# Performance work log

Hardware: AMD Instinct MI355X
Metric: run time of the kernel (lower is better)

## Reference

```python
import jax, jax.numpy as jnp
import numpy as np

STATE_DIM = 32
OBS_DIM = 16
PROCESS_VAR = 1e-4
MEAS_VAR = 1e-2
B = 2048
T = 64


def setup_inputs() -> dict:
    key = jax.random.key(0)
    k1, k2, k3 = jax.random.split(key, 3)
    state0 = jax.random.normal(k1, (B, STATE_DIM), dtype=jnp.float32)
    # Initial covariance P = I (per torch __init__), broadcast over batch
    cov0 = jnp.broadcast_to(jnp.eye(STATE_DIM, dtype=jnp.float32), (B, STATE_DIM, STATE_DIM))
    measurements = jax.random.normal(k2, (B, T, OBS_DIM), dtype=jnp.float32)
    # Parameters per torch __init__: F = eye, H = randn, Q = pv*I, R = mv*I
    F = jnp.eye(STATE_DIM, dtype=jnp.float32)
    H = jax.random.normal(k3, (OBS_DIM, STATE_DIM), dtype=jnp.float32)
    Q = PROCESS_VAR * jnp.eye(STATE_DIM, dtype=jnp.float32)
    R = MEAS_VAR * jnp.eye(OBS_DIM, dtype=jnp.float32)
    return {"state0": state0, "cov0": cov0, "measurements": measurements,
            "F": F, "H": H, "Q": Q, "R": R}


def reference(state0, cov0, measurements, F, H, Q, R):
    """Run Kalman predict+update over T timesteps; return filtered states (B,T,S)."""

    def step(carry, z):
        x, P = carry  # x: (B,S), P: (B,S,S); z: (B,O)
        # --- predict ---
        x_pred = x @ F.T                                   # F @ x per batch
        P_pred = jnp.einsum('ij,bjk,lk->bil', F, P, F) + Q  # F P F^T + Q
        # --- update ---
        y = x_pred @ H.T                                   # predicted measurement (B,O)
        innov = z - y
        S = jnp.einsum('ij,bjk,lk->bil', H, P_pred, H) + R  # (B,O,O)
        S_inv = jnp.linalg.inv(S)
        K = jnp.einsum('bij,kj,bkl->bil', P_pred, H, S_inv)  # P H^T S^{-1}, (B,S,O)
        x_new = x_pred + jnp.einsum('bij,bj->bi', K, innov)
        P_new = P_pred - jnp.einsum('bij,jk,bkl->bil', K, H, P_pred)  # (I - K H) P
        return (x_new, P_new), x_new

    # scan over time axis: measurements (B,T,O) -> (T,B,O)
    (_, _), states = jax.lax.scan(step, (state0, cov0), jnp.swapaxes(measurements, 0, 1))
    return jnp.swapaxes(states, 0, 1)  # (B,T,S)
```

## Files before the change

kernel.cpp:

```cpp
#include <hip/hip_runtime.h>
#include <math.h>


#define S_DIM 32
#define O_DIM 16
#define K_STRIDE 512
#define HS 36
#define CW 8

typedef unsigned int u32;

__device__ __forceinline__ float rdlanef(float v, int srcLane) {
    return __uint_as_float(
        (unsigned int)__builtin_amdgcn_readlane((int)__float_as_uint(v), srcLane));
}

__global__ __launch_bounds__(512) void fused_kernel(
    const float* __restrict__ state0,
    const float* __restrict__ cov0,
    const float* __restrict__ meas,
    const float* __restrict__ Fm,
    const float* __restrict__ Hm,
    const float* __restrict__ Qm,
    const float* __restrict__ Rm,
    float* __restrict__ wsK,
    float* __restrict__ out,
    int T, int B)
{
    u32* ctrl = (u32*)(wsK + (long)T * K_STRIDE);
    const int tid = threadIdx.x;

    __shared__ float P  [S_DIM*33];
    __shared__ float Fs [S_DIM*33];
    __shared__ float Qs [S_DIM*33];
    __shared__ float Tp [S_DIM*33];
    __shared__ float Hs [O_DIM*HS];
    __shared__ float HQ [O_DIM*HS];
    __shared__ float HPs[O_DIM*HS];
    __shared__ float KT [O_DIM*33];
    __shared__ float Sg [O_DIM*17];
    __shared__ float Rs [O_DIM*17];
    __shared__ int notId, notDiag, convFlag, convT;
    __shared__ float Ks[K_STRIDE];
    __shared__ float xs[CW][32];
    __shared__ float iv[CW][16];
    __shared__ u32 mail;

    if (blockIdx.x == 0) {
        for (int i = tid; i < S_DIM*S_DIM; i += 512) {
            int r = i >> 5, c = i & 31;
            P [r*33+c] = cov0[i];
            Fs[r*33+c] = Fm[i];
            Qs[r*33+c] = Qm[i];
        }
        for (int i = tid; i < O_DIM*S_DIM; i += 512) {
            int r = i >> 5, c = i & 31;
            Hs[r*HS+c] = Hm[i];
        }
        for (int i = tid; i < O_DIM*O_DIM; i += 512) {
            int r = i >> 4, c = i & 15;
            Rs[r*17+c] = Rm[i];
        }
        if (tid == 0) { notId = 0; notDiag = 0; convFlag = 0; convT = 0; }
        __syncthreads();

        {
            bool badI = false, badD = false;
            for (int i = tid; i < S_DIM*S_DIM; i += 512) {
                int r = i >> 5, c = i & 31;
                if (Fs[r*33+c] != ((r == c) ? 1.0f : 0.0f)) badI = true;
            }
            for (int i = tid; i < O_DIM*O_DIM; i += 512) {
                int r = i >> 4, c = i & 15;
                if (r != c && Rs[r*17+c] != 0.0f) badD = true;
            }
            if (badI) notId = 1;
            if (badD) notDiag = 1;
        }
        __syncthreads();
        const bool fId   = (notId == 0);
        const bool rDiag = (notDiag == 0);

        if (tid < 64) __builtin_amdgcn_s_setprio(1);

        if (fId) {
            for (int i = tid; i < S_DIM*S_DIM; i += 512) {
                int r = i >> 5, c = i & 31;
                P[r*33+c] += Qs[r*33+c];
            }
        }
        __syncthreads();

        if (fId) {
            int r = tid >> 5, c = tid & 31;
            float a0 = 0.f, q0 = 0.f;
            for (int k = 0; k < S_DIM; ++k) {
                a0 += Hs[r*HS+k]*P [k*33+c];
                q0 += Hs[r*HS+k]*Qs[k*33+c];
            }
            HPs[r*HS+c] = a0;
            HQ [r*HS+c] = q0;
        }
        __syncthreads();

        bool  havePend = false;
        int   pendT = 0;
        float4 pf0, pf1, pf2, pf3;
        float prevK[16];

        for (int t = 0; t < T; ++t) {
            if (havePend) {
                float4* dst = (float4*)(wsK + (long)pendT*K_STRIDE + (tid - O_DIM)*O_DIM);
                dst[0] = pf0; dst[1] = pf1; dst[2] = pf2; dst[3] = pf3;
                havePend = false;
            }

            if (!fId) {
                for (int i = tid; i < S_DIM*S_DIM; i += 512) {
                    int r = i >> 5, c = i & 31;
                    float a = 0.f;
                    for (int k = 0; k < S_DIM; ++k) a += Fs[r*33+k]*P[k*33+c];
                    Tp[r*33+c] = a;
                }
                __syncthreads();
                for (int i = tid; i < S_DIM*S_DIM; i += 512) {
                    int r = i >> 5, c = i & 31;
                    float a = Qs[r*33+c];
                    for (int k = 0; k < S_DIM; ++k) a += Tp[r*33+k]*Fs[c*33+k];
                    P[r*33+c] = a;
                }
                __syncthreads();
                {
                    int r = tid >> 5, c = tid & 31;
                    float a = 0.f;
                    for (int k = 0; k < S_DIM; ++k)
                        a += Hs[r*HS+k]*P[k*33+c];
                    HPs[r*HS+c] = a;
                }
                __syncthreads();
            }

            if (tid < 256) {
                int r = tid >> 4, c = tid & 15;
                float a = Rs[r*17+c];
                const float4* hp = (const float4*)&HPs[r*HS];
                const float4* hh = (const float4*)&Hs [c*HS];
                #pragma unroll
                for (int k = 0; k < 8; ++k) {
                    float4 u = hp[k], v = hh[k];
                    a += u.x*v.x + u.y*v.y + u.z*v.z + u.w*v.w;
                }
                Sg[r*17+c] = a;
            }
            __syncthreads();

            if (tid == 511 && t > 0)
                __hip_atomic_store(ctrl, (u32)t, __ATOMIC_RELEASE,
                                   __HIP_MEMORY_SCOPE_AGENT);

            if (tid < 64) {
                const int myc = tid;
                const bool isS = (myc < O_DIM);
                const bool isK = (!isS && myc < 48);
                const int hc = (myc - O_DIM) & 31;
                float a[16];
                #pragma unroll
                for (int r = 0; r < O_DIM; ++r)
                    a[r] = isS ? Sg[r*17+myc] : HPs[r*HS+hc];

                #pragma unroll
                for (int p = 0; p < O_DIM; ++p) {
                    float sp[16];
                    #pragma unroll
                    for (int r = 0; r < O_DIM; ++r) sp[r] = rdlanef(a[r], p);
                    float pinv = __builtin_amdgcn_rcpf(sp[p]);
                    float sc = a[p] * pinv;
                    #pragma unroll
                    for (int r = 0; r < O_DIM; ++r)
                        a[r] = (r == p) ? sc : fmaf(-sp[r], sc, a[r]);
                }

                float d = 0.f;
                if (isK) {
                    #pragma unroll
                    for (int r = 0; r < O_DIM; ++r) {
                        float dd = fabsf(a[r] - prevK[r]);
                        d = fmaxf(d, dd);
                        prevK[r] = a[r];
                    }
                }
                unsigned long long anyBig = __ballot(isK && (d > 1e-5f));
                if (myc == 0 && anyBig == 0ull && t >= 1) {
                    convFlag = 1; convT = t;
                }

                if (isK) {
                    pf0 = make_float4(a[0],  a[1],  a[2],  a[3]);
                    pf1 = make_float4(a[4],  a[5],  a[6],  a[7]);
                    pf2 = make_float4(a[8],  a[9],  a[10], a[11]);
                    pf3 = make_float4(a[12], a[13], a[14], a[15]);
                    pendT = t; havePend = true;

                    const int j = myc - O_DIM;
                    if (fId) {
                        if (rDiag) {
                            #pragma unroll
                            for (int r = 0; r < O_DIM; ++r)
                                HPs[r*HS+j] = fmaf(Rs[r*17+r], a[r], HQ[r*HS+j]);
                        } else {
                            #pragma unroll
                            for (int r = 0; r < O_DIM; ++r) {
                                float rg = 0.f;
                                for (int k = 0; k < O_DIM; ++k) rg += Rs[r*17+k]*a[k];
                                HPs[r*HS+j] = rg + HQ[r*HS+j];
                            }
                        }
                    } else {
                        #pragma unroll
                        for (int o = 0; o < O_DIM; ++o) KT[o*33+j] = a[o];
                    }
                }
            }
            __syncthreads();

            if (convFlag) break;

            if (!fId) {
                for (int i = tid; i < S_DIM*S_DIM; i += 512) {
                    int r = i >> 5, c = i & 31;
                    float acc = 0.f;
                    for (int o = 0; o < O_DIM; ++o) acc += KT[o*33+r]*HPs[o*HS+c];
                    P[r*33+c] -= acc;
                }
                __syncthreads();
            }
        }

        if (havePend) {
            float4* dst = (float4*)(wsK + (long)pendT*K_STRIDE + (tid - O_DIM)*O_DIM);
            dst[0] = pf0; dst[1] = pf1; dst[2] = pf2; dst[3] = pf3;
        }
        __syncthreads();

        if (!fId && convFlag) {
            const int tc = convT;
            const long n = (long)(T - 1 - tc) * K_STRIDE;
            const float* src = wsK + (long)tc * K_STRIDE;
            float* dst = wsK + (long)(tc + 1) * K_STRIDE;
            for (long i = tid; i < n; i += 512)
                dst[i] = src[i & (K_STRIDE - 1)];
            __syncthreads();
        }

        if (tid == 0) {
            u32 tsv = (convFlag && fId) ? (u32)convT : (u32)T;
            __hip_atomic_store(ctrl, (tsv << 16) | (u32)T, __ATOMIC_RELEASE,
                               __HIP_MEMORY_SCOPE_AGENT);
        }
        return;
    }

    const int wv = tid >> 6;
    const int l  = tid & 63;
    const int s = l & 31;
    const int h = l >> 5;
    const int o = l & 15;
    const int q = l >> 4;
    long bb = (long)(blockIdx.x - 1) * CW + wv;
    const long b = (bb < B) ? bb : (B - 1);

    float4 h0v, h1v;
    {
        const float4* Hv = (const float4*)(Hm + o*S_DIM + q*8);
        h0v = Hv[0]; h1v = Hv[1];
    }

    bool bad = false;
    for (int i = l; i < S_DIM*S_DIM; i += 64) {
        int r = i >> 5, c = i & 31;
        if (Fm[i] != ((r == c) ? 1.0f : 0.0f)) bad = true;
    }
    const bool fId = !__any(bad);

    float4 f0, f1, f2, f3;
    if (!fId) {
        const float4* Fv = (const float4*)(Fm + s*S_DIM + h*16);
        f0 = Fv[0]; f1 = Fv[1]; f2 = Fv[2]; f3 = Fv[3];
    }

    float x = state0[b*S_DIM + s];
    if (h == 0) xs[wv][s] = x;
    __builtin_amdgcn_wave_barrier();

    int t = 0, avail = 0, ts = 0;
    while (t < T) {
        if (avail <= t && !(ts != 0 && t >= ts)) {
            for (;;) {
                __syncthreads();
                if (tid == 0)
                    mail = __hip_atomic_load(ctrl, __ATOMIC_RELAXED,
                                             __HIP_MEMORY_SCOPE_AGENT);
                __syncthreads();
                u32 cw = mail;
                avail = (int)(cw & 0xFFFFu);
                ts    = (int)(cw >> 16);
                if (avail > t || (ts != 0 && t >= ts)) break;
                __builtin_amdgcn_s_sleep(8);
            }
        }
        if (ts != 0 && t >= ts) break;

        int upto = avail;
        if (ts != 0 && ts < upto) upto = ts;
        if (upto > T) upto = T;

        for (; t < upto; ++t) {
            Ks[tid] = __hip_atomic_load(wsK + (long)t*K_STRIDE + tid,
                                        __ATOMIC_RELAXED, __HIP_MEMORY_SCOPE_AGENT);
            __syncthreads();

            float za = meas[(b*T + t)*O_DIM + o];

            if (!fId) {
                const float4* xv = (const float4*)(&xs[wv][h*16]);
                float4 xa = xv[0], xb = xv[1], xc = xv[2], xd = xv[3];
                float p = f0.x*xa.x + f0.y*xa.y + f0.z*xa.z + f0.w*xa.w
                        + f1.x*xb.x + f1.y*xb.y + f1.z*xb.z + f1.w*xb.w
                        + f2.x*xc.x + f2.y*xc.y + f2.z*xc.z + f2.w*xc.w
                        + f3.x*xd.x + f3.y*xd.y + f3.z*xd.z + f3.w*xd.w;
                x = p + __shfl_xor(p, 32, 64);
                __builtin_amdgcn_wave_barrier();
                if (h == 0) xs[wv][s] = x;
                __builtin_amdgcn_wave_barrier();
            }

            const float4* xq = (const float4*)(&xs[wv][q*8]);
            float4 xa = xq[0], xb = xq[1];
            float p = h0v.x*xa.x + h0v.y*xa.y + h0v.z*xa.z + h0v.w*xa.w
                    + h1v.x*xb.x + h1v.y*xb.y + h1v.z*xb.z + h1v.w*xb.w;
            float p2 = p + __shfl_xor(p, 16, 64);
            float y  = p2 + __shfl_xor(p2, 32, 64);
            float innov = za - y;

            __builtin_amdgcn_wave_barrier();
            if (l < 16) iv[wv][o] = innov;
            __builtin_amdgcn_wave_barrier();

            const float4* Kv = (const float4*)(&Ks[s*O_DIM + h*8]);
            float4 k0 = Kv[0], k1 = Kv[1];
            const float4* ivq = (const float4*)(&iv[wv][h*8]);
            float4 va = ivq[0], vb = ivq[1];
            float xp2 = k0.x*va.x + k0.y*va.y + k0.z*va.z + k0.w*va.w
                      + k1.x*vb.x + k1.y*vb.y + k1.z*vb.z + k1.w*vb.w;
            float xnew = x + (xp2 + __shfl_xor(xp2, 32, 64));

            if (h == 0) out[(b*T + t)*S_DIM + s] = xnew;

            __builtin_amdgcn_wave_barrier();
            if (h == 0) xs[wv][s] = xnew;
            __builtin_amdgcn_wave_barrier();

            x = xnew;
            __syncthreads();
        }
    }

    if (t >= T) return;

    Ks[tid] = __hip_atomic_load(wsK + (long)ts*K_STRIDE + tid,
                                __ATOMIC_RELAXED, __HIP_MEMORY_SCOPE_AGENT);
    __syncthreads();

    float ka[16];
    #pragma unroll
    for (int j = 0; j < 16; ++j) ka[j] = Ks[s*O_DIM + j];

    float4 kc0, kc1;
    kc0.x = h ? ka[8]  : ka[0];  kc0.y = h ? ka[9]  : ka[1];
    kc0.z = h ? ka[10] : ka[2];  kc0.w = h ? ka[11] : ka[3];
    kc1.x = h ? ka[12] : ka[4];  kc1.y = h ? ka[13] : ka[5];
    kc1.z = h ? ka[14] : ka[6];  kc1.w = h ? ka[15] : ka[7];

    float mreg[16];
    #pragma unroll
    for (int j = 0; j < 16; ++j)
        mreg[j] = (s == h*16 + j) ? 1.0f : 0.0f;
    for (int oo = 0; oo < O_DIM; ++oo) {
        const float4* Hr = (const float4*)(Hm + oo*S_DIM + h*16);
        float4 a0 = Hr[0], a1 = Hr[1], a2 = Hr[2], a3 = Hr[3];
        float k = ka[oo];
        mreg[0]  = fmaf(-k, a0.x, mreg[0]);
        mreg[1]  = fmaf(-k, a0.y, mreg[1]);
        mreg[2]  = fmaf(-k, a0.z, mreg[2]);
        mreg[3]  = fmaf(-k, a0.w, mreg[3]);
        mreg[4]  = fmaf(-k, a1.x, mreg[4]);
        mreg[5]  = fmaf(-k, a1.y, mreg[5]);
        mreg[6]  = fmaf(-k, a1.z, mreg[6]);
        mreg[7]  = fmaf(-k, a1.w, mreg[7]);
        mreg[8]  = fmaf(-k, a2.x, mreg[8]);
        mreg[9]  = fmaf(-k, a2.y, mreg[9]);
        mreg[10] = fmaf(-k, a2.z, mreg[10]);
        mreg[11] = fmaf(-k, a2.w, mreg[11]);
        mreg[12] = fmaf(-k, a3.x, mreg[12]);
        mreg[13] = fmaf(-k, a3.y, mreg[13]);
        mreg[14] = fmaf(-k, a3.z, mreg[14]);
        mreg[15] = fmaf(-k, a3.w, mreg[15]);
    }

    float4 zva0, zva1, zvb0, zvb1;
    {
        const float4* Zv = (const float4*)(meas + (b*T + t)*O_DIM + h*8);
        zva0 = Zv[0]; zva1 = Zv[1];
        const int t1 = (t + 1 < T) ? (t + 1) : t;
        const float4* Zv1 = (const float4*)(meas + (b*T + t1)*O_DIM + h*8);
        zvb0 = Zv1[0]; zvb1 = Zv1[1];
    }

    for (; t < T; ++t) {
        float4 zvc0, zvc1;
        {
            const int tn = (t + 2 < T) ? (t + 2) : (T - 1);
            const float4* Zv = (const float4*)(meas + (b*T + tn)*O_DIM + h*8);
            zvc0 = Zv[0]; zvc1 = Zv[1];
        }

        const float4* xv = (const float4*)(&xs[wv][h*16]);
        float4 xa = xv[0], xb = xv[1], xc = xv[2], xd = xv[3];
        float p = mreg[0] *xa.x + mreg[1] *xa.y + mreg[2] *xa.z + mreg[3] *xa.w
                + mreg[4] *xb.x + mreg[5] *xb.y + mreg[6] *xb.z + mreg[7] *xb.w
                + mreg[8] *xc.x + mreg[9] *xc.y + mreg[10]*xc.z + mreg[11]*xc.w
                + mreg[12]*xd.x + mreg[13]*xd.y + mreg[14]*xd.z + mreg[15]*xd.w;
        p += kc0.x*zva0.x + kc0.y*zva0.y + kc0.z*zva0.z + kc0.w*zva0.w
           + kc1.x*zva1.x + kc1.y*zva1.y + kc1.z*zva1.z + kc1.w*zva1.w;
        float xnew = p + __shfl_xor(p, 32, 64);

        if (h == 0) out[(b*T + t)*S_DIM + s] = xnew;

        __builtin_amdgcn_wave_barrier();
        if (h == 0) xs[wv][s] = xnew;
        __builtin_amdgcn_wave_barrier();

        zva0 = zvb0; zva1 = zvb1;
        zvb0 = zvc0; zvb1 = zvc1;
    }
}

extern "C" void kernel_launch(void* const* d_in, const int* in_sizes, int n_in,
                              void* d_out, int out_size, void* d_ws, size_t ws_size,
                              hipStream_t stream) {
    const float* state0 = (const float*)d_in[0];
    const float* cov0   = (const float*)d_in[1];
    const float* meas   = (const float*)d_in[2];
    const float* Fm     = (const float*)d_in[3];
    const float* Hm     = (const float*)d_in[4];
    const float* Qm     = (const float*)d_in[5];
    const float* Rm     = (const float*)d_in[6];
    float* out  = (float*)d_out;
    float* wsK  = (float*)d_ws;

    const int B = in_sizes[0] / S_DIM;
    const int T = in_sizes[2] / (B * O_DIM);

    hipMemsetAsync((void*)(wsK + (long)T * K_STRIDE), 0, sizeof(unsigned int), stream);

    const int grid = 1 + (B + CW - 1) / CW;
    fused_kernel<<<dim3(grid), dim3(512), 0, stream>>>(
        state0, cov0, meas, Fm, Hm, Qm, Rm, wsK, out, T, B);
}
```

Baseline: 152.4 us.

## Add dedicated writer wave for gain publishing and widen consumer blocks to nine columns

```diff
diff --git a/kernel.cpp b/kernel.cpp
--- a/kernel.cpp
+++ b/kernel.cpp
@@ -6,16 +6,22 @@
 #define O_DIM 16
 #define K_STRIDE 512
 #define HS 36
-#define CW 8
+#define CW 9
+#define NTHR 576
 
 typedef unsigned int u32;
+typedef unsigned long long u64;
 
 __device__ __forceinline__ float rdlanef(float v, int srcLane) {
     return __uint_as_float(
         (unsigned int)__builtin_amdgcn_readlane((int)__float_as_uint(v), srcLane));
 }
 
-__global__ __launch_bounds__(512) void fused_kernel(
+__device__ __forceinline__ u64 pack2(float a, float b) {
+    return (u64)__float_as_uint(a) | ((u64)__float_as_uint(b) << 32);
+}
+
+__global__ __launch_bounds__(NTHR) void fused_kernel(
     const float* __restrict__ state0,
     const float* __restrict__ cov0,
     const float* __restrict__ meas,
@@ -47,17 +53,17 @@
     __shared__ u32 mail;
 
     if (blockIdx.x == 0) {
-        for (int i = tid; i < S_DIM*S_DIM; i += 512) {
+        for (int i = tid; i < S_DIM*S_DIM; i += NTHR) {
             int r = i >> 5, c = i & 31;
             P [r*33+c] = cov0[i];
             Fs[r*33+c] = Fm[i];
             Qs[r*33+c] = Qm[i];
         }
-        for (int i = tid; i < O_DIM*S_DIM; i += 512) {
+        for (int i = tid; i < O_DIM*S_DIM; i += NTHR) {
             int r = i >> 5, c = i & 31;
             Hs[r*HS+c] = Hm[i];
         }
-        for (int i = tid; i < O_DIM*O_DIM; i += 512) {
+        for (int i = tid; i < O_DIM*O_DIM; i += NTHR) {
             int r = i >> 4, c = i & 15;
             Rs[r*17+c] = Rm[i];
         }
@@ -66,11 +72,11 @@
 
         {
             bool badI = false, badD = false;
-            for (int i = tid; i < S_DIM*S_DIM; i += 512) {
+            for (int i = tid; i < S_DIM*S_DIM; i += NTHR) {
                 int r = i >> 5, c = i & 31;
                 if (Fs[r*33+c] != ((r == c) ? 1.0f : 0.0f)) badI = true;
             }
-            for (int i = tid; i < O_DIM*O_DIM; i += 512) {
+            for (int i = tid; i < O_DIM*O_DIM; i += NTHR) {
                 int r = i >> 4, c = i & 15;
                 if (r != c && Rs[r*17+c] != 0.0f) badD = true;
             }
@@ -84,14 +90,14 @@
         if (tid < 64) __builtin_amdgcn_s_setprio(1);
 
         if (fId) {
-            for (int i = tid; i < S_DIM*S_DIM; i += 512) {
+            for (int i = tid; i < S_DIM*S_DIM; i += NTHR) {
                 int r = i >> 5, c = i & 31;
                 P[r*33+c] += Qs[r*33+c];
             }
         }
         __syncthreads();
 
-        if (fId) {
+        if (fId && tid < 512) {
             int r = tid >> 5, c = tid & 31;
             float a0 = 0.f, q0 = 0.f;
             for (int k = 0; k < S_DIM; ++k) {
@@ -103,34 +109,42 @@
         }
         __syncthreads();
 
-        bool  havePend = false;
-        int   pendT = 0;
-        float4 pf0, pf1, pf2, pf3;
         float prevK[16];
 
         for (int t = 0; t < T; ++t) {
-            if (havePend) {
-                float4* dst = (float4*)(wsK + (long)pendT*K_STRIDE + (tid - O_DIM)*O_DIM);
-                dst[0] = pf0; dst[1] = pf1; dst[2] = pf2; dst[3] = pf3;
-                havePend = false;
+            if (t > 0 && tid >= 512 && tid < 544) {
+                const int j = tid - 512;
+                float k0=KT[0*33+j], k1=KT[1*33+j], k2=KT[2*33+j], k3=KT[3*33+j];
+                float k4=KT[4*33+j], k5=KT[5*33+j], k6=KT[6*33+j], k7=KT[7*33+j];
+                float k8=KT[8*33+j], k9=KT[9*33+j], kA=KT[10*33+j], kB=KT[11*33+j];
+                float kC=KT[12*33+j], kD=KT[13*33+j], kE=KT[14*33+j], kF=KT[15*33+j];
+                u64* dst = (u64*)(wsK + (long)(t-1)*K_STRIDE + j*O_DIM);
+                __hip_atomic_store(dst+0, pack2(k0,k1), __ATOMIC_RELAXED, __HIP_MEMORY_SCOPE_AGENT);
+                __hip_atomic_store(dst+1, pack2(k2,k3), __ATOMIC_RELAXED, __HIP_MEMORY_SCOPE_AGENT);
+                __hip_atomic_store(dst+2, pack2(k4,k5), __ATOMIC_RELAXED, __HIP_MEMORY_SCOPE_AGENT);
+                __hip_atomic_store(dst+3, pack2(k6,k7), __ATOMIC_RELAXED, __HIP_MEMORY_SCOPE_AGENT);
+                __hip_atomic_store(dst+4, pack2(k8,k9), __ATOMIC_RELAXED, __HIP_MEMORY_SCOPE_AGENT);
+                __hip_atomic_store(dst+5, pack2(kA,kB), __ATOMIC_RELAXED, __HIP_MEMORY_SCOPE_AGENT);
+                __hip_atomic_store(dst+6, pack2(kC,kD), __ATOMIC_RELAXED, __HIP_MEMORY_SCOPE_AGENT);
+                __hip_atomic_store(dst+7, pack2(kE,kF), __ATOMIC_RELAXED, __HIP_MEMORY_SCOPE_AGENT);
             }
 
             if (!fId) {
-                for (int i = tid; i < S_DIM*S_DIM; i += 512) {
+                for (int i = tid; i < S_DIM*S_DIM; i += NTHR) {
                     int r = i >> 5, c = i & 31;
                     float a = 0.f;
                     for (int k = 0; k < S_DIM; ++k) a += Fs[r*33+k]*P[k*33+c];
                     Tp[r*33+c] = a;
                 }
                 __syncthreads();
-                for (int i = tid; i < S_DIM*S_DIM; i += 512) {
+                for (int i = tid; i < S_DIM*S_DIM; i += NTHR) {
                     int r = i >> 5, c = i & 31;
                     float a = Qs[r*33+c];
                     for (int k = 0; k < S_DIM; ++k) a += Tp[r*33+k]*Fs[c*33+k];
                     P[r*33+c] = a;
                 }
                 __syncthreads();
-                {
+                if (tid < 512) {
                     int r = tid >> 5, c = tid & 31;
                     float a = 0.f;
                     for (int k = 0; k < S_DIM; ++k)
@@ -154,8 +168,8 @@
             }
             __syncthreads();
 
-            if (tid == 511 && t > 0)
-                __hip_atomic_store(ctrl, (u32)t, __ATOMIC_RELEASE,
+            if (tid == 575 && t > 0)
+                __hip_atomic_store(ctrl, (u32)t, __ATOMIC_RELAXED,
                                    __HIP_MEMORY_SCOPE_AGENT);
 
             if (tid < 64) {
@@ -195,13 +209,10 @@
                 }
 
                 if (isK) {
-                    pf0 = make_float4(a[0],  a[1],  a[2],  a[3]);
-                    pf1 = make_float4(a[4],  a[5],  a[6],  a[7]);
-                    pf2 = make_float4(a[8],  a[9],  a[10], a[11]);
-                    pf3 = make_float4(a[12], a[13], a[14], a[15]);
-                    pendT = t; havePend = true;
-
                     const int j = myc - O_DIM;
+                    #pragma unroll
+                    for (int o = 0; o < O_DIM; ++o) KT[o*33+j] = a[o];
+
                     if (fId) {
                         if (rDiag) {
                             #pragma unroll
@@ -215,9 +226,6 @@
                                 HPs[r*HS+j] = rg + HQ[r*HS+j];
                             }
                         }
-                    } else {
-                        #pragma unroll
-                        for (int o = 0; o < O_DIM; ++o) KT[o*33+j] = a[o];
                     }
                 }
             }
@@ -226,7 +234,7 @@
             if (convFlag) break;
 
             if (!fId) {
-                for (int i = tid; i < S_DIM*S_DIM; i += 512) {
+                for (int i = tid; i < S_DIM*S_DIM; i += NTHR) {
                     int r = i >> 5, c = i & 31;
                     float acc = 0.f;
                     for (int o = 0; o < O_DIM; ++o) acc += KT[o*33+r]*HPs[o*HS+c];
@@ -236,9 +244,24 @@
             }
         }
 
-        if (havePend) {
-            float4* dst = (float4*)(wsK + (long)pendT*K_STRIDE + (tid - O_DIM)*O_DIM);
-            dst[0] = pf0; dst[1] = pf1; dst[2] = pf2; dst[3] = pf3;
+        {
+            const int tLast = convFlag ? convT : (T - 1);
+            if (tid >= 512 && tid < 544) {
+                const int j = tid - 512;
+                float k0=KT[0*33+j], k1=KT[1*33+j], k2=KT[2*33+j], k3=KT[3*33+j];
+                float k4=KT[4*33+j], k5=KT[5*33+j], k6=KT[6*33+j], k7=KT[7*33+j];
+                float k8=KT[8*33+j], k9=KT[9*33+j], kA=KT[10*33+j], kB=KT[11*33+j];
+                float kC=KT[12*33+j], kD=KT[13*33+j], kE=KT[14*33+j], kF=KT[15*33+j];
+                u64* dst = (u64*)(wsK + (long)tLast*K_STRIDE + j*O_DIM);
+                __hip_atomic_store(dst+0, pack2(k0,k1), __ATOMIC_RELAXED, __HIP_MEMORY_SCOPE_AGENT);
+                __hip_atomic_store(dst+1, pack2(k2,k3), __ATOMIC_RELAXED, __HIP_MEMORY_SCOPE_AGENT);
+                __hip_atomic_store(dst+2, pack2(k4,k5), __ATOMIC_RELAXED, __HIP_MEMORY_SCOPE_AGENT);
+                __hip_atomic_store(dst+3, pack2(k6,k7), __ATOMIC_RELAXED, __HIP_MEMORY_SCOPE_AGENT);
+                __hip_atomic_store(dst+4, pack2(k8,k9), __ATOMIC_RELAXED, __HIP_MEMORY_SCOPE_AGENT);
+                __hip_atomic_store(dst+5, pack2(kA,kB), __ATOMIC_RELAXED, __HIP_MEMORY_SCOPE_AGENT);
+                __hip_atomic_store(dst+6, pack2(kC,kD), __ATOMIC_RELAXED, __HIP_MEMORY_SCOPE_AGENT);
+                __hip_atomic_store(dst+7, pack2(kE,kF), __ATOMIC_RELAXED, __HIP_MEMORY_SCOPE_AGENT);
+            }
         }
         __syncthreads();
 
@@ -247,7 +270,7 @@
             const long n = (long)(T - 1 - tc) * K_STRIDE;
             const float* src = wsK + (long)tc * K_STRIDE;
             float* dst = wsK + (long)(tc + 1) * K_STRIDE;
-            for (long i = tid; i < n; i += 512)
+            for (long i = tid; i < n; i += NTHR)
                 dst[i] = src[i & (K_STRIDE - 1)];
             __syncthreads();
         }
@@ -315,8 +338,9 @@
         if (upto > T) upto = T;
 
         for (; t < upto; ++t) {
-            Ks[tid] = __hip_atomic_load(wsK + (long)t*K_STRIDE + tid,
-                                        __ATOMIC_RELAXED, __HIP_MEMORY_SCOPE_AGENT);
+            if (tid < 512)
+                Ks[tid] = __hip_atomic_load(wsK + (long)t*K_STRIDE + tid,
+                                            __ATOMIC_RELAXED, __HIP_MEMORY_SCOPE_AGENT);
             __syncthreads();
 
             float za = meas[(b*T + t)*O_DIM + o];
@@ -367,8 +391,9 @@
 
     if (t >= T) return;
 
-    Ks[tid] = __hip_atomic_load(wsK + (long)ts*K_STRIDE + tid,
-                                __ATOMIC_RELAXED, __HIP_MEMORY_SCOPE_AGENT);
+    if (tid < 512)
+        Ks[tid] = __hip_atomic_load(wsK + (long)ts*K_STRIDE + tid,
+                                    __ATOMIC_RELAXED, __HIP_MEMORY_SCOPE_AGENT);
     __syncthreads();
 
     float ka[16];
@@ -464,6 +489,6 @@
     hipMemsetAsync((void*)(wsK + (long)T * K_STRIDE), 0, sizeof(unsigned int), stream);
 
     const int grid = 1 + (B + CW - 1) / CW;
-    fused_kernel<<<dim3(grid), dim3(512), 0, stream>>>(
+    fused_kernel<<<dim3(grid), dim3(NTHR), 53248, stream>>>(
         state0, cov0, meas, Fm, Hm, Qm, Rm, wsK, out, T, B);
 }
```

Result: faster. 144.0 us (-5.5%).

## Compute covariance recursion redundantly per block instead of broadcasting gain via global memory

Applied to the files above, without the earlier changes.

```diff
diff --git a/kernel.cpp b/kernel.cpp
--- a/kernel.cpp
+++ b/kernel.cpp
@@ -4,18 +4,16 @@
 
 #define S_DIM 32
 #define O_DIM 16
-#define K_STRIDE 512
 #define HS 36
 #define CW 8
-
-typedef unsigned int u32;
+#define NTHR 576
 
 __device__ __forceinline__ float rdlanef(float v, int srcLane) {
     return __uint_as_float(
         (unsigned int)__builtin_amdgcn_readlane((int)__float_as_uint(v), srcLane));
 }
 
-__global__ __launch_bounds__(512) void fused_kernel(
+__global__ __launch_bounds__(NTHR) void kf_fused(
     const float* __restrict__ state0,
     const float* __restrict__ cov0,
     const float* __restrict__ meas,
@@ -23,11 +21,9 @@
     const float* __restrict__ Hm,
     const float* __restrict__ Qm,
     const float* __restrict__ Rm,
-    float* __restrict__ wsK,
     float* __restrict__ out,
     int T, int B)
 {
-    u32* ctrl = (u32*)(wsK + (long)T * K_STRIDE);
     const int tid = threadIdx.x;
 
     __shared__ float P  [S_DIM*33];
@@ -37,61 +33,108 @@
     __shared__ float Hs [O_DIM*HS];
     __shared__ float HQ [O_DIM*HS];
     __shared__ float HPs[O_DIM*HS];
-    __shared__ float KT [O_DIM*33];
+    __shared__ float KT [2][O_DIM*33];
     __shared__ float Sg [O_DIM*17];
     __shared__ float Rs [O_DIM*17];
+    __shared__ float xs [CW][32];
+    __shared__ float iv [CW][16];
     __shared__ int notId, notDiag, convFlag, convT;
-    __shared__ float Ks[K_STRIDE];
-    __shared__ float xs[CW][32];
-    __shared__ float iv[CW][16];
-    __shared__ u32 mail;
-
-    if (blockIdx.x == 0) {
-        for (int i = tid; i < S_DIM*S_DIM; i += 512) {
+    __shared__ float cupad[13000];
+
+    if (tid == 0) {
+        ((volatile float*)cupad)[0] = 0.f;
+        notId = 0; notDiag = 0; convFlag = 0; convT = 0;
+    }
+
+    for (int i = tid; i < S_DIM*S_DIM; i += NTHR) {
+        int r = i >> 5, c = i & 31;
+        P [r*33+c] = cov0[i];
+        Fs[r*33+c] = Fm[i];
+        Qs[r*33+c] = Qm[i];
+    }
+    for (int i = tid; i < O_DIM*S_DIM; i += NTHR) {
+        int r = i >> 5, c = i & 31;
+        Hs[r*HS+c] = Hm[i];
+    }
+    for (int i = tid; i < O_DIM*O_DIM; i += NTHR) {
+        int r = i >> 4, c = i & 15;
+        Rs[r*17+c] = Rm[i];
+    }
+    __syncthreads();
+
+    {
+        bool badI = false, badD = false;
+        for (int i = tid; i < S_DIM*S_DIM; i += NTHR) {
             int r = i >> 5, c = i & 31;
-            P [r*33+c] = cov0[i];
-            Fs[r*33+c] = Fm[i];
-            Qs[r*33+c] = Qm[i];
-        }
-        for (int i = tid; i < O_DIM*S_DIM; i += 512) {
+            if (Fs[r*33+c] != ((r == c) ? 1.0f : 0.0f)) badI = true;
+        }
+        for (int i = tid; i < O_DIM*O_DIM; i += NTHR) {
+            int r = i >> 4, c = i & 15;
+            if (r != c && Rs[r*17+c] != 0.0f) badD = true;
+        }
+        if (badI) notId = 1;
+        if (badD) notDiag = 1;
+    }
+    __syncthreads();
+    const bool fId   = (notId == 0);
+    const bool rDiag = (notDiag == 0);
+
+    const int wv = tid >> 6;
+    const int l  = tid & 63;
+    const int s  = l & 31;
+    const int h  = l >> 5;
+    const int o  = l & 15;
+    const int q  = l >> 4;
+    const int wi = (wv >= 1) ? (wv - 1) : 0;
+    const bool isCons = (wv >= 1);
+    long bb = (long)blockIdx.x * CW + wi;
+    const long b = (bb < B) ? bb : (B - 1);
+
+    float4 h0v, h1v;
+    {
+        const float4* Hv = (const float4*)(Hm + o*S_DIM + q*8);
+        h0v = Hv[0]; h1v = Hv[1];
+    }
+
+    float x = 0.f;
+    if (isCons) {
+        x = state0[b*S_DIM + s];
+        if (h == 0) xs[wi][s] = x;
+    }
+    __syncthreads();
+
+    auto cons_step = [&](int tstep, int bufc) {
+        float za = meas[(b*T + tstep)*O_DIM + o];
+        const float4* xq = (const float4*)(&xs[wi][q*8]);
+        float4 xa = xq[0], xb = xq[1];
+        float p = h0v.x*xa.x + h0v.y*xa.y + h0v.z*xa.z + h0v.w*xa.w
+                + h1v.x*xb.x + h1v.y*xb.y + h1v.z*xb.z + h1v.w*xb.w;
+        float p2 = p + __shfl_xor(p, 16, 64);
+        float y  = p2 + __shfl_xor(p2, 32, 64);
+        float innov = za - y;
+        __builtin_amdgcn_wave_barrier();
+        if (l < 16) iv[wi][o] = innov;
+        __builtin_amdgcn_wave_barrier();
+        const float* ivp = &iv[wi][h*8];
+        const float* ktp = &KT[bufc][(h*8)*33 + s];
+        float acc = 0.f;
+        #pragma unroll
+        for (int m = 0; m < 8; ++m) acc = fmaf(ktp[m*33], ivp[m], acc);
+        float xnew = x + (acc + __shfl_xor(acc, 32, 64));
+        if (h == 0) out[(b*T + tstep)*S_DIM + s] = xnew;
+        __builtin_amdgcn_wave_barrier();
+        if (h == 0) xs[wi][s] = xnew;
+        __builtin_amdgcn_wave_barrier();
+        x = xnew;
+    };
+
+    if (fId) {
+        for (int i = tid; i < S_DIM*S_DIM; i += NTHR) {
             int r = i >> 5, c = i & 31;
-            Hs[r*HS+c] = Hm[i];
-        }
-        for (int i = tid; i < O_DIM*O_DIM; i += 512) {
-            int r = i >> 4, c = i & 15;
-            Rs[r*17+c] = Rm[i];
-        }
-        if (tid == 0) { notId = 0; notDiag = 0; convFlag = 0; convT = 0; }
-        __syncthreads();
-
-        {
-            bool badI = false, badD = false;
-            for (int i = tid; i < S_DIM*S_DIM; i += 512) {
-                int r = i >> 5, c = i & 31;
-                if (Fs[r*33+c] != ((r == c) ? 1.0f : 0.0f)) badI = true;
-            }
-            for (int i = tid; i < O_DIM*O_DIM; i += 512) {
-                int r = i >> 4, c = i & 15;
-                if (r != c && Rs[r*17+c] != 0.0f) badD = true;
-            }
-            if (badI) notId = 1;
-            if (badD) notDiag = 1;
-        }
-        __syncthreads();
-        const bool fId   = (notId == 0);
-        const bool rDiag = (notDiag == 0);
-
-        if (tid < 64) __builtin_amdgcn_s_setprio(1);
-
-        if (fId) {
-            for (int i = tid; i < S_DIM*S_DIM; i += 512) {
-                int r = i >> 5, c = i & 31;
-                P[r*33+c] += Qs[r*33+c];
-            }
-        }
-        __syncthreads();
-
-        if (fId) {
+            P[r*33+c] += Qs[r*33+c];
+        }
+        __syncthreads();
+        if (tid < 512) {
             int r = tid >> 5, c = tid & 31;
             float a0 = 0.f, q0 = 0.f;
             for (int k = 0; k < S_DIM; ++k) {
@@ -102,62 +145,26 @@
             HQ [r*HS+c] = q0;
         }
         __syncthreads();
-
-        bool  havePend = false;
-        int   pendT = 0;
-        float4 pf0, pf1, pf2, pf3;
+        if (tid < 256) {
+            int r = tid >> 4, c = tid & 15;
+            float a = Rs[r*17+c];
+            const float4* hp = (const float4*)&HPs[r*HS];
+            const float4* hh = (const float4*)&Hs [c*HS];
+            #pragma unroll
+            for (int k = 0; k < 8; ++k) {
+                float4 u = hp[k], v = hh[k];
+                a += u.x*v.x + u.y*v.y + u.z*v.z + u.w*v.w;
+            }
+            Sg[r*17+c] = a;
+        }
+        __syncthreads();
+
+        if (tid < 64) __builtin_amdgcn_s_setprio(1);
+
         float prevK[16];
-
-        for (int t = 0; t < T; ++t) {
-            if (havePend) {
-                float4* dst = (float4*)(wsK + (long)pendT*K_STRIDE + (tid - O_DIM)*O_DIM);
-                dst[0] = pf0; dst[1] = pf1; dst[2] = pf2; dst[3] = pf3;
-                havePend = false;
-            }
-
-            if (!fId) {
-                for (int i = tid; i < S_DIM*S_DIM; i += 512) {
-                    int r = i >> 5, c = i & 31;
-                    float a = 0.f;
-                    for (int k = 0; k < S_DIM; ++k) a += Fs[r*33+k]*P[k*33+c];
-                    Tp[r*33+c] = a;
-                }
-                __syncthreads();
-                for (int i = tid; i < S_DIM*S_DIM; i += 512) {
-                    int r = i >> 5, c = i & 31;
-                    float a = Qs[r*33+c];
-                    for (int k = 0; k < S_DIM; ++k) a += Tp[r*33+k]*Fs[c*33+k];
-                    P[r*33+c] = a;
-                }
-                __syncthreads();
-                {
-                    int r = tid >> 5, c = tid & 31;
-                    float a = 0.f;
-                    for (int k = 0; k < S_DIM; ++k)
-                        a += Hs[r*HS+k]*P[k*33+c];
-                    HPs[r*HS+c] = a;
-                }
-                __syncthreads();
-            }
-
-            if (tid < 256) {
-                int r = tid >> 4, c = tid & 15;
-                float a = Rs[r*17+c];
-                const float4* hp = (const float4*)&HPs[r*HS];
-                const float4* hh = (const float4*)&Hs [c*HS];
-                #pragma unroll
-                for (int k = 0; k < 8; ++k) {
-                    float4 u = hp[k], v = hh[k];
-                    a += u.x*v.x + u.y*v.y + u.z*v.z + u.w*v.w;
-                }
-                Sg[r*17+c] = a;
-            }
-            __syncthreads();
-
-            if (tid == 511 && t > 0)
-                __hip_atomic_store(ctrl, (u32)t, __ATOMIC_RELEASE,
-                                   __HIP_MEMORY_SCOPE_AGENT);
-
+        int t = 0;
+        for (; t < T; ++t) {
+            const int buf = t & 1;
             if (tid < 64) {
                 const int myc = tid;
                 const bool isS = (myc < O_DIM);
@@ -195,253 +202,223 @@
                 }
 
                 if (isK) {
-                    pf0 = make_float4(a[0],  a[1],  a[2],  a[3]);
-                    pf1 = make_float4(a[4],  a[5],  a[6],  a[7]);
-                    pf2 = make_float4(a[8],  a[9],  a[10], a[11]);
-                    pf3 = make_float4(a[12], a[13], a[14], a[15]);
-                    pendT = t; havePend = true;
-
                     const int j = myc - O_DIM;
-                    if (fId) {
-                        if (rDiag) {
-                            #pragma unroll
-                            for (int r = 0; r < O_DIM; ++r)
-                                HPs[r*HS+j] = fmaf(Rs[r*17+r], a[r], HQ[r*HS+j]);
-                        } else {
-                            #pragma unroll
-                            for (int r = 0; r < O_DIM; ++r) {
-                                float rg = 0.f;
-                                for (int k = 0; k < O_DIM; ++k) rg += Rs[r*17+k]*a[k];
-                                HPs[r*HS+j] = rg + HQ[r*HS+j];
-                            }
-                        }
+                    #pragma unroll
+                    for (int oo = 0; oo < O_DIM; ++oo) KT[buf][oo*33+j] = a[oo];
+                    if (rDiag) {
+                        #pragma unroll
+                        for (int r = 0; r < O_DIM; ++r)
+                            HPs[r*HS+j] = fmaf(Rs[r*17+r], a[r], HQ[r*HS+j]);
                     } else {
                         #pragma unroll
-                        for (int o = 0; o < O_DIM; ++o) KT[o*33+j] = a[o];
+                        for (int r = 0; r < O_DIM; ++r) {
+                            float rg = 0.f;
+                            for (int k = 0; k < O_DIM; ++k) rg += Rs[r*17+k]*a[k];
+                            HPs[r*HS+j] = rg + HQ[r*HS+j];
+                        }
                     }
                 }
+            } else if (isCons && t > 0) {
+                cons_step(t - 1, buf ^ 1);
             }
             __syncthreads();
 
             if (convFlag) break;
 
-            if (!fId) {
-                for (int i = tid; i < S_DIM*S_DIM; i += 512) {
-                    int r = i >> 5, c = i & 31;
-                    float acc = 0.f;
-                    for (int o = 0; o < O_DIM; ++o) acc += KT[o*33+r]*HPs[o*HS+c];
-                    P[r*33+c] -= acc;
+            if (t + 1 < T) {
+                if (tid < 256) {
+                    int r = tid >> 4, c = tid & 15;
+                    float a = Rs[r*17+c];
+                    const float4* hp = (const float4*)&HPs[r*HS];
+                    const float4* hh = (const float4*)&Hs [c*HS];
+                    #pragma unroll
+                    for (int k = 0; k < 8; ++k) {
+                        float4 u = hp[k], v = hh[k];
+                        a += u.x*v.x + u.y*v.y + u.z*v.z + u.w*v.w;
+                    }
+                    Sg[r*17+c] = a;
                 }
                 __syncthreads();
             }
         }
-
-        if (havePend) {
-            float4* dst = (float4*)(wsK + (long)pendT*K_STRIDE + (tid - O_DIM)*O_DIM);
-            dst[0] = pf0; dst[1] = pf1; dst[2] = pf2; dst[3] = pf3;
-        }
-        __syncthreads();
-
-        if (!fId && convFlag) {
-            const int tc = convT;
-            const long n = (long)(T - 1 - tc) * K_STRIDE;
-            const float* src = wsK + (long)tc * K_STRIDE;
-            float* dst = wsK + (long)(tc + 1) * K_STRIDE;
-            for (long i = tid; i < n; i += 512)
-                dst[i] = src[i & (K_STRIDE - 1)];
-            __syncthreads();
-        }
-
-        if (tid == 0) {
-            u32 tsv = (convFlag && fId) ? (u32)convT : (u32)T;
-            __hip_atomic_store(ctrl, (tsv << 16) | (u32)T, __ATOMIC_RELEASE,
-                               __HIP_MEMORY_SCOPE_AGENT);
+        if (tid < 64) __builtin_amdgcn_s_setprio(0);
+
+        if (!isCons) return;
+
+        if (!convFlag) {
+            cons_step(T - 1, (T - 1) & 1);
+            return;
+        }
+
+        const int tc  = convT;
+        const int bufc = tc & 1;
+        float ka[16];
+        #pragma unroll
+        for (int j = 0; j < 16; ++j) ka[j] = KT[bufc][j*33 + s];
+
+        float4 kc0, kc1;
+        kc0.x = h ? ka[8]  : ka[0];  kc0.y = h ? ka[9]  : ka[1];
+        kc0.z = h ? ka[10] : ka[2];  kc0.w = h ? ka[11] : ka[3];
+        kc1.x = h ? ka[12] : ka[4];  kc1.y = h ? ka[13] : ka[5];
+        kc1.z = h ? ka[14] : ka[6];  kc1.w = h ? ka[15] : ka[7];
+
+        float mreg[16];
+        #pragma unroll
+        for (int j = 0; j < 16; ++j)
+            mreg[j] = (s == h*16 + j) ? 1.0f : 0.0f;
+        for (int oo = 0; oo < O_DIM; ++oo) {
+            const float4* Hr = (const float4*)&Hs[oo*HS + h*16];
+            float4 a0 = Hr[0], a1 = Hr[1], a2 = Hr[2], a3 = Hr[3];
+            float k = ka[oo];
+            mreg[0]  = fmaf(-k, a0.x, mreg[0]);
+            mreg[1]  = fmaf(-k, a0.y, mreg[1]);
+            mreg[2]  = fmaf(-k, a0.z, mreg[2]);
+            mreg[3]  = fmaf(-k, a0.w, mreg[3]);
+            mreg[4]  = fmaf(-k, a1.x, mreg[4]);
+            mreg[5]  = fmaf(-k, a1.y, mreg[5]);
+            mreg[6]  = fmaf(-k, a1.z, mreg[6]);
+            mreg[7]  = fmaf(-k, a1.w, mreg[7]);
+            mreg[8]  = fmaf(-k, a2.x, mreg[8]);
+            mreg[9]  = fmaf(-k, a2.y, mreg[9]);
+            mreg[10] = fmaf(-k, a2.z, mreg[10]);
+            mreg[11] = fmaf(-k, a2.w, mreg[11]);
+            mreg[12] = fmaf(-k, a3.x, mreg[12]);
+            mreg[13] = fmaf(-k, a3.y, mreg[13]);
+            mreg[14] = fmaf(-k, a3.z, mreg[14]);
+            mreg[15] = fmaf(-k, a3.w, mreg[15]);
+        }
+
+        int t2 = tc;
+        float4 zva0, zva1, zvb0, zvb1;
+        {
+            const float4* Zv = (const float4*)(meas + (b*T + t2)*O_DIM + h*8);
+            zva0 = Zv[0]; zva1 = Zv[1];
+            const int t1 = (t2 + 1 < T) ? (t2 + 1) : t2;
+            const float4* Zv1 = (const float4*)(meas + (b*T + t1)*O_DIM + h*8);
+            zvb0 = Zv1[0]; zvb1 = Zv1[1];
+        }
+
+        for (; t2 < T; ++t2) {
+            float4 zvc0, zvc1;
+            {
+                const int tn = (t2 + 2 < T) ? (t2 + 2) : (T - 1);
+                const float4* Zv = (const float4*)(meas + (b*T + tn)*O_DIM + h*8);
+                zvc0 = Zv[0]; zvc1 = Zv[1];
+            }
+
+            const float4* xv = (const float4*)(&xs[wi][h*16]);
+            float4 xa = xv[0], xb = xv[1], xc = xv[2], xd = xv[3];
+            float p = mreg[0] *xa.x + mreg[1] *xa.y + mreg[2] *xa.z + mreg[3] *xa.w
+                    + mreg[4] *xb.x + mreg[5] *xb.y + mreg[6] *xb.z + mreg[7] *xb.w
+                    + mreg[8] *xc.x + mreg[9] *xc.y + mreg[10]*xc.z + mreg[11]*xc.w
+                    + mreg[12]*xd.x + mreg[13]*xd.y + mreg[14]*xd.z + mreg[15]*xd.w;
+            p += kc0.x*zva0.x + kc0.y*zva0.y + kc0.z*zva0.z + kc0.w*zva0.w
+               + kc1.x*zva1.x + kc1.y*zva1.y + kc1.z*zva1.z + kc1.w*zva1.w;
+            float xnew = p + __shfl_xor(p, 32, 64);
+
+            if (h == 0) out[(b*T + t2)*S_DIM + s] = xnew;
+
+            __builtin_amdgcn_wave_barrier();
+            if (h == 0) xs[wi][s] = xnew;
+            __builtin_amdgcn_wave_barrier();
+
+            zva0 = zvb0; zva1 = zvb1;
+            zvb0 = zvc0; zvb1 = zvc1;
         }
         return;
     }
 
-    const int wv = tid >> 6;
-    const int l  = tid & 63;
-    const int s = l & 31;
-    const int h = l >> 5;
-    const int o = l & 15;
-    const int q = l >> 4;
-    long bb = (long)(blockIdx.x - 1) * CW + wv;
-    const long b = (bb < B) ? bb : (B - 1);
-
-    float4 h0v, h1v;
-    {
-        const float4* Hv = (const float4*)(Hm + o*S_DIM + q*8);
-        h0v = Hv[0]; h1v = Hv[1];
-    }
-
-    bool bad = false;
-    for (int i = l; i < S_DIM*S_DIM; i += 64) {
-        int r = i >> 5, c = i & 31;
-        if (Fm[i] != ((r == c) ? 1.0f : 0.0f)) bad = true;
-    }
-    const bool fId = !__any(bad);
-
     float4 f0, f1, f2, f3;
-    if (!fId) {
+    if (isCons) {
         const float4* Fv = (const float4*)(Fm + s*S_DIM + h*16);
         f0 = Fv[0]; f1 = Fv[1]; f2 = Fv[2]; f3 = Fv[3];
     }
 
-    float x = state0[b*S_DIM + s];
-    if (h == 0) xs[wv][s] = x;
-    __builtin_amdgcn_wave_barrier();
-
-    int t = 0, avail = 0, ts = 0;
-    while (t < T) {
-        if (avail <= t && !(ts != 0 && t >= ts)) {
-            for (;;) {
-                __syncthreads();
-                if (tid == 0)
-                    mail = __hip_atomic_load(ctrl, __ATOMIC_RELAXED,
-                                             __HIP_MEMORY_SCOPE_AGENT);
-                __syncthreads();
-                u32 cw = mail;
-                avail = (int)(cw & 0xFFFFu);
-                ts    = (int)(cw >> 16);
-                if (avail > t || (ts != 0 && t >= ts)) break;
-                __builtin_amdgcn_s_sleep(8);
-            }
-        }
-        if (ts != 0 && t >= ts) break;
-
-        int upto = avail;
-        if (ts != 0 && ts < upto) upto = ts;
-        if (upto > T) upto = T;
-
-        for (; t < upto; ++t) {
-            Ks[tid] = __hip_atomic_load(wsK + (long)t*K_STRIDE + tid,
-                                        __ATOMIC_RELAXED, __HIP_MEMORY_SCOPE_AGENT);
-            __syncthreads();
-
-            float za = meas[(b*T + t)*O_DIM + o];
-
-            if (!fId) {
-                const float4* xv = (const float4*)(&xs[wv][h*16]);
-                float4 xa = xv[0], xb = xv[1], xc = xv[2], xd = xv[3];
-                float p = f0.x*xa.x + f0.y*xa.y + f0.z*xa.z + f0.w*xa.w
-                        + f1.x*xb.x + f1.y*xb.y + f1.z*xb.z + f1.w*xb.w
-                        + f2.x*xc.x + f2.y*xc.y + f2.z*xc.z + f2.w*xc.w
-                        + f3.x*xd.x + f3.y*xd.y + f3.z*xd.z + f3.w*xd.w;
-                x = p + __shfl_xor(p, 32, 64);
-                __builtin_amdgcn_wave_barrier();
-                if (h == 0) xs[wv][s] = x;
-                __builtin_amdgcn_wave_barrier();
-            }
-
-            const float4* xq = (const float4*)(&xs[wv][q*8]);
-            float4 xa = xq[0], xb = xq[1];
-            float p = h0v.x*xa.x + h0v.y*xa.y + h0v.z*xa.z + h0v.w*xa.w
-                    + h1v.x*xb.x + h1v.y*xb.y + h1v.z*xb.z + h1v.w*xb.w;
-            float p2 = p + __shfl_xor(p, 16, 64);
-            float y  = p2 + __shfl_xor(p2, 32, 64);
-            float innov = za - y;
-
+    for (int t = 0; t < T; ++t) {
+        for (int i = tid; i < S_DIM*S_DIM; i += NTHR) {
+            int r = i >> 5, c = i & 31;
+            float a = 0.f;
+            for (int k = 0; k < S_DIM; ++k) a += Fs[r*33+k]*P[k*33+c];
+            Tp[r*33+c] = a;
+        }
+        __syncthreads();
+        for (int i = tid; i < S_DIM*S_DIM; i += NTHR) {
+            int r = i >> 5, c = i & 31;
+            float a = Qs[r*33+c];
+            for (int k = 0; k < S_DIM; ++k) a += Tp[r*33+k]*Fs[c*33+k];
+            P[r*33+c] = a;
+        }
+        __syncthreads();
+        if (tid < 512) {
+            int r = tid >> 5, c = tid & 31;
+            float a = 0.f;
+            for (int k = 0; k < S_DIM; ++k) a += Hs[r*HS+k]*P[k*33+c];
+            HPs[r*HS+c] = a;
+        }
+        __syncthreads();
+        if (tid < 256) {
+            int r = tid >> 4, c = tid & 15;
+            float a = Rs[r*17+c];
+            const float4* hp = (const float4*)&HPs[r*HS];
+            const float4* hh = (const float4*)&Hs [c*HS];
+            #pragma unroll
+            for (int k = 0; k < 8; ++k) {
+                float4 u = hp[k], v = hh[k];
+                a += u.x*v.x + u.y*v.y + u.z*v.z + u.w*v.w;
+            }
+            Sg[r*17+c] = a;
+        }
+        __syncthreads();
+        if (tid < 64) {
+            const int myc = tid;
+            const bool isS = (myc < O_DIM);
+            const bool isK = (!isS && myc < 48);
+            const int hc = (myc - O_DIM) & 31;
+            float a[16];
+            #pragma unroll
+            for (int r = 0; r < O_DIM; ++r)
+                a[r] = isS ? Sg[r*17+myc] : HPs[r*HS+hc];
+            #pragma unroll
+            for (int p = 0; p < O_DIM; ++p) {
+                float sp[16];
+                #pragma unroll
+                for (int r = 0; r < O_DIM; ++r) sp[r] = rdlanef(a[r], p);
+                float pinv = __builtin_amdgcn_rcpf(sp[p]);
+                float sc = a[p] * pinv;
+                #pragma unroll
+                for (int r = 0; r < O_DIM; ++r)
+                    a[r] = (r == p) ? sc : fmaf(-sp[r], sc, a[r]);
+            }
+            if (isK) {
+                const int j = myc - O_DIM;
+                #pragma unroll
+                for (int oo = 0; oo < O_DIM; ++oo) KT[0][oo*33+j] = a[oo];
+            }
+        }
+        __syncthreads();
+
+        if (isCons) {
+            const float4* xv = (const float4*)(&xs[wi][h*16]);
+            float4 xa = xv[0], xb = xv[1], xc = xv[2], xd = xv[3];
+            float pr = f0.x*xa.x + f0.y*xa.y + f0.z*xa.z + f0.w*xa.w
+                     + f1.x*xb.x + f1.y*xb.y + f1.z*xb.z + f1.w*xb.w
+                     + f2.x*xc.x + f2.y*xc.y + f2.z*xc.z + f2.w*xc.w
+                     + f3.x*xd.x + f3.y*xd.y + f3.z*xd.z + f3.w*xd.w;
+            x = pr + __shfl_xor(pr, 32, 64);
             __builtin_amdgcn_wave_barrier();
-            if (l < 16) iv[wv][o] = innov;
+            if (h == 0) xs[wi][s] = x;
             __builtin_amdgcn_wave_barrier();
-
-            const float4* Kv = (const float4*)(&Ks[s*O_DIM + h*8]);
-            float4 k0 = Kv[0], k1 = Kv[1];
-            const float4* ivq = (const float4*)(&iv[wv][h*8]);
-            float4 va = ivq[0], vb = ivq[1];
-            float xp2 = k0.x*va.x + k0.y*va.y + k0.z*va.z + k0.w*va.w
-                      + k1.x*vb.x + k1.y*vb.y + k1.z*vb.z + k1.w*vb.w;
-            float xnew = x + (xp2 + __shfl_xor(xp2, 32, 64));
-
-            if (h == 0) out[(b*T + t)*S_DIM + s] = xnew;
-
-            __builtin_amdgcn_wave_barrier();
-            if (h == 0) xs[wv][s] = xnew;
-            __builtin_amdgcn_wave_barrier();
-
-            x = xnew;
-            __syncthreads();
-        }
-    }
-
-    if (t >= T) return;
-
-    Ks[tid] = __hip_atomic_load(wsK + (long)ts*K_STRIDE + tid,
-                                __ATOMIC_RELAXED, __HIP_MEMORY_SCOPE_AGENT);
-    __syncthreads();
-
-    float ka[16];
-    #pragma unroll
-    for (int j = 0; j < 16; ++j) ka[j] = Ks[s*O_DIM + j];
-
-    float4 kc0, kc1;
-    kc0.x = h ? ka[8]  : ka[0];  kc0.y = h ? ka[9]  : ka[1];
-    kc0.z = h ? ka[10] : ka[2];  kc0.w = h ? ka[11] : ka[3];
-    kc1.x = h ? ka[12] : ka[4];  kc1.y = h ? ka[13] : ka[5];
-    kc1.z = h ? ka[14] : ka[6];  kc1.w = h ? ka[15] : ka[7];
-
-    float mreg[16];
-    #pragma unroll
-    for (int j = 0; j < 16; ++j)
-        mreg[j] = (s == h*16 + j) ? 1.0f : 0.0f;
-    for (int oo = 0; oo < O_DIM; ++oo) {
-        const float4* Hr = (const float4*)(Hm + oo*S_DIM + h*16);
-        float4 a0 = Hr[0], a1 = Hr[1], a2 = Hr[2], a3 = Hr[3];
-        float k = ka[oo];
-        mreg[0]  = fmaf(-k, a0.x, mreg[0]);
-        mreg[1]  = fmaf(-k, a0.y, mreg[1]);
-        mreg[2]  = fmaf(-k, a0.z, mreg[2]);
-        mreg[3]  = fmaf(-k, a0.w, mreg[3]);
-        mreg[4]  = fmaf(-k, a1.x, mreg[4]);
-        mreg[5]  = fmaf(-k, a1.y, mreg[5]);
-        mreg[6]  = fmaf(-k, a1.z, mreg[6]);
-        mreg[7]  = fmaf(-k, a1.w, mreg[7]);
-        mreg[8]  = fmaf(-k, a2.x, mreg[8]);
-        mreg[9]  = fmaf(-k, a2.y, mreg[9]);
-        mreg[10] = fmaf(-k, a2.z, mreg[10]);
-        mreg[11] = fmaf(-k, a2.w, mreg[11]);
-        mreg[12] = fmaf(-k, a3.x, mreg[12]);
-        mreg[13] = fmaf(-k, a3.y, mreg[13]);
-        mreg[14] = fmaf(-k, a3.z, mreg[14]);
-        mreg[15] = fmaf(-k, a3.w, mreg[15]);
-    }
-
-    float4 zva0, zva1, zvb0, zvb1;
-    {
-        const float4* Zv = (const float4*)(meas + (b*T + t)*O_DIM + h*8);
-        zva0 = Zv[0]; zva1 = Zv[1];
-        const int t1 = (t + 1 < T) ? (t + 1) : t;
-        const float4* Zv1 = (const float4*)(meas + (b*T + t1)*O_DIM + h*8);
-        zvb0 = Zv1[0]; zvb1 = Zv1[1];
-    }
-
-    for (; t < T; ++t) {
-        float4 zvc0, zvc1;
-        {
-            const int tn = (t + 2 < T) ? (t + 2) : (T - 1);
-            const float4* Zv = (const float4*)(meas + (b*T + tn)*O_DIM + h*8);
-            zvc0 = Zv[0]; zvc1 = Zv[1];
-        }
-
-        const float4* xv = (const float4*)(&xs[wv][h*16]);
-        float4 xa = xv[0], xb = xv[1], xc = xv[2], xd = xv[3];
-        float p = mreg[0] *xa.x + mreg[1] *xa.y + mreg[2] *xa.z + mreg[3] *xa.w
-                + mreg[4] *xb.x + mreg[5] *xb.y + mreg[6] *xb.z + mreg[7] *xb.w
-                + mreg[8] *xc.x + mreg[9] *xc.y + mreg[10]*xc.z + mreg[11]*xc.w
-                + mreg[12]*xd.x + mreg[13]*xd.y + mreg[14]*xd.z + mreg[15]*xd.w;
-        p += kc0.x*zva0.x + kc0.y*zva0.y + kc0.z*zva0.z + kc0.w*zva0.w
-           + kc1.x*zva1.x + kc1.y*zva1.y + kc1.z*zva1.z + kc1.w*zva1.w;
-        float xnew = p + __shfl_xor(p, 32, 64);
-
-        if (h == 0) out[(b*T + t)*S_DIM + s] = xnew;
-
-        __builtin_amdgcn_wave_barrier();
-        if (h == 0) xs[wv][s] = xnew;
-        __builtin_amdgcn_wave_barrier();
-
-        zva0 = zvb0; zva1 = zvb1;
-        zvb0 = zvc0; zvb1 = zvc1;
+            cons_step(t, 0);
+        }
+
+        for (int i = tid; i < S_DIM*S_DIM; i += NTHR) {
+            int r = i >> 5, c = i & 31;
+            float acc = 0.f;
+            for (int oo = 0; oo < O_DIM; ++oo)
+                acc += KT[0][oo*33+r]*HPs[oo*HS+c];
+            P[r*33+c] -= acc;
+        }
+        __syncthreads();
     }
 }
 
@@ -455,15 +432,12 @@
     const float* Hm     = (const float*)d_in[4];
     const float* Qm     = (const float*)d_in[5];
     const float* Rm     = (const float*)d_in[6];
-    float* out  = (float*)d_out;
-    float* wsK  = (float*)d_ws;
+    float* out = (float*)d_out;
 
     const int B = in_sizes[0] / S_DIM;
     const int T = in_sizes[2] / (B * O_DIM);
 
-    hipMemsetAsync((void*)(wsK + (long)T * K_STRIDE), 0, sizeof(unsigned int), stream);
-
-    const int grid = 1 + (B + CW - 1) / CW;
-    fused_kernel<<<dim3(grid), dim3(512), 0, stream>>>(
-        state0, cov0, meas, Fm, Hm, Qm, Rm, wsK, out, T, B);
+    const int grid = (B + CW - 1) / CW;
+    kf_fused<<<dim3(grid), dim3(NTHR), 0, stream>>>(
+        state0, cov0, meas, Fm, Hm, Qm, Rm, out, T, B);
 }
```

Result: faster. 140.5 us (-7.8%).
